# Kernel tuning notes

Hardware: AMD Instinct MI355X
Metric: run time of the kernel (lower is better)

The kernel has to match this reference:

```python
import jax, jax.numpy as jnp
import numpy as np


def setup_inputs() -> dict:
    key = jax.random.key(0)
    ks = jax.random.split(key, 16)
    B, S, D, H = 32, 2048, 512, 512
    s = 1.0 / np.sqrt(H)
    inp = {
        "x": jax.random.normal(ks[0], (B, H), jnp.float32),
        "context": jax.random.normal(ks[1], (B, S, D), jnp.float32),
        "mask": jnp.zeros((B, S), jnp.bool_),  # False = valid position
        "Wi": jax.random.normal(ks[2], (H, H), jnp.float32) * s,
        "bi": jax.random.normal(ks[3], (H,), jnp.float32) * s,
        "Wc0": jax.random.normal(ks[4], (H, D), jnp.float32) * s,
        "bc0": jax.random.normal(ks[5], (H,), jnp.float32) * s,
        "Wc1": jax.random.normal(ks[6], (H, D), jnp.float32) * s,
        "bc1": jax.random.normal(ks[7], (H,), jnp.float32) * s,
        "Wc2": jax.random.normal(ks[8], (H, D), jnp.float32) * s,
        "bc2": jax.random.normal(ks[9], (H,), jnp.float32) * s,
        "Wc3": jax.random.normal(ks[10], (H, D), jnp.float32) * s,
        "bc3": jax.random.normal(ks[11], (H,), jnp.float32) * s,
        "V": jax.random.uniform(ks[12], (H,), jnp.float32, -s, s),
    }
    return inp


def reference(x, context, mask, Wi, bi, Wc0, bc0, Wc1, bc1, Wc2, bc2, Wc3, bc3, V):
    # mask: True = masked out in the original API; module flips it first.
    valid = ~mask  # [B, S], True = keep

    inp = (x @ Wi.T + bi)[:, :, None]  # [B, H, 1]

    def proj(W, b):
        # Conv1d(D, H, kernel=1) on context.permute(0,2,1) == token-wise GEMM
        return jnp.einsum("bsd,hd->bhs", context, W) + b[None, :, None]  # [B, H, S]

    ctx = jnp.concatenate(
        [proj(Wc0, bc0), proj(Wc1, bc1), proj(Wc2, bc2), proj(Wc3, bc3)], axis=2
    )  # [B, H, 4S]

    t = jnp.tanh(inp + ctx)                      # [B, H, 4S]
    att = jnp.einsum("h,bhs->bs", V, t)          # bmm(V[B,1,H], t).squeeze(1)
    att = 10.0 * jnp.tanh(att)                   # [B, 4S]

    valid4 = jnp.tile(valid, (1, 4))             # mask.repeat(1, 4)
    att = jnp.where(valid4, att, -jnp.inf)
    # torch.no_grad() around the masked fill detaches the rest of the graph
    att = jax.lax.stop_gradient(att)

    ans = jax.nn.softmax(att, axis=1)            # [B, 4S]
    p = jnp.max(ans, axis=1)
    indices = jnp.argmax(ans, axis=1)
    return indices[:, None], p[:, None], mask
```

## Files before the change

kernel.cpp:

```cpp
#include <hip/hip_runtime.h>
#include <math.h>

typedef __bf16 bf16x8 __attribute__((ext_vector_type(8)));
typedef float f32x4 __attribute__((ext_vector_type(4)));
typedef short short8v __attribute__((ext_vector_type(8)));

#define MARGIN 0.01f
#define NCAND 32

#define WAITL  do { asm volatile("s_waitcnt lgkmcnt(0)" ::: "memory"); __builtin_amdgcn_sched_barrier(0); } while (0)
#define WAITV0 do { asm volatile("s_waitcnt vmcnt(0)" ::: "memory"); __builtin_amdgcn_sched_barrier(0); } while (0)
#define BARR   do { __builtin_amdgcn_s_barrier(); __builtin_amdgcn_sched_barrier(0); } while (0)

__device__ __forceinline__ unsigned short f2bf(float f) {
  unsigned u = __float_as_uint(f);
  u += 0x7fffu + ((u >> 16) & 1u);
  return (unsigned short)(u >> 16);
}
__device__ __forceinline__ float tanh_fast(float x) {
  float e = __builtin_amdgcn_exp2f(x * 2.885390081777927f);
  return 1.f - 2.f * __builtin_amdgcn_rcpf(e + 1.f);
}
__device__ __forceinline__ void gl_lds16(const void* g, void* l) {
  __builtin_amdgcn_global_load_lds(
      (const __attribute__((address_space(1))) unsigned int*)g,
      (__attribute__((address_space(3))) unsigned int*)l, 16, 0, 0);
}
__device__ __forceinline__ float dpp_row_reduce(float v) {
  int x;
  x = __builtin_amdgcn_update_dpp(0, __builtin_bit_cast(int, v), 0x118, 0xf, 0xf, true);
  v += __builtin_bit_cast(float, x);
  x = __builtin_amdgcn_update_dpp(0, __builtin_bit_cast(int, v), 0x114, 0xf, 0xf, true);
  v += __builtin_bit_cast(float, x);
  x = __builtin_amdgcn_update_dpp(0, __builtin_bit_cast(int, v), 0x112, 0xf, 0xf, true);
  v += __builtin_bit_cast(float, x);
  x = __builtin_amdgcn_update_dpp(0, __builtin_bit_cast(int, v), 0x111, 0xf, 0xf, true);
  v += __builtin_bit_cast(float, x);
  return v;
}

__global__ __launch_bounds__(256) void prep_all_k(
    const float* __restrict__ ctx, const float* __restrict__ x,
    const float* __restrict__ Wi, const float* __restrict__ bi,
    const float* __restrict__ w0, const float* __restrict__ w1,
    const float* __restrict__ w2, const float* __restrict__ w3,
    short* __restrict__ Chi, short* __restrict__ Whi, float* __restrict__ inp,
    int ctx_blocks) {
  int bid = blockIdx.x;
  if (bid < ctx_blocks) {
    int gid = bid * 256 + threadIdx.x;
    int c = gid & 3, row = (gid >> 2) & 127, TK = gid >> 9;
    int MT = TK >> 4, KS = TK & 15;
    size_t m = (size_t)MT * 128 + row;
    int k = KS * 32 + c * 8;
    float f[8];
    *(float4*)&f[0] = *(const float4*)(ctx + m * 512 + k);
    *(float4*)&f[4] = *(const float4*)(ctx + m * 512 + k + 4);
    short8v hv;
    #pragma unroll
    for (int i = 0; i < 8; ++i) hv[i] = (short)f2bf(f[i]);
    *(short8v*)(Chi + (size_t)gid * 8) = hv;
  } else if (bid < ctx_blocks + 512) {
    int gid = (bid - ctx_blocks) * 256 + threadIdx.x;
    int c = gid & 3, row = (gid >> 2) & 511, TK = gid >> 11;
    int TN = TK >> 4, KS = TK & 15;
    const float* w = (TN == 0) ? w0 : (TN == 1) ? w1 : (TN == 2) ? w2 : w3;
    const float* src = w + (size_t)row * 512 + KS * 32 + c * 8;
    float f[8];
    *(float4*)&f[0] = *(const float4*)(src);
    *(float4*)&f[4] = *(const float4*)(src + 4);
    short8v hv;
    #pragma unroll
    for (int i = 0; i < 8; ++i) hv[i] = (short)f2bf(f[i]);
    *(short8v*)(Whi + (size_t)gid * 8) = hv;
  } else {
    int gid = (bid - ctx_blocks - 512) * 256 + threadIdx.x;
    int b = gid >> 9, h = gid & 511;
    const float* xr = x + b * 512;
    const float* wr = Wi + h * 512;
    float acc = bi[h];
    #pragma unroll 4
    for (int k = 0; k < 512; k += 4) {
      float4 xv = *(const float4*)(xr + k);
      float4 wv = *(const float4*)(wr + k);
      acc += xv.x * wv.x + xv.y * wv.y + xv.z * wv.z + xv.w * wv.w;
    }
    inp[gid] = acc;
  }
}

template<bool PRESPLIT>
__global__ __launch_bounds__(1024, 4) void gemm_att_k(
    const float* __restrict__ ctx, const short* __restrict__ Chi,
    const short* __restrict__ Whi,
    const float* __restrict__ inp,
    const float* __restrict__ bc0, const float* __restrict__ bc1,
    const float* __restrict__ bc2, const float* __restrict__ bc3,
    const float* __restrict__ V, float* __restrict__ att) {
  __shared__ __align__(16) short smem[2][20480];

  const int t = threadIdx.x;
  int d = blockIdx.x + (blockIdx.y << 3);
  int work = (d & 7) * 256 + (d >> 3);
  int mt = work >> 2, nt = work & 3;
  int b = mt >> 4;
  const float* bc = (nt == 0) ? bc0 : (nt == 1) ? bc1 : (nt == 2) ? bc2 : bc3;

  auto stageA = [&](int tile, int slot) {
    if (t < 512)
      gl_lds16(Chi + (((size_t)mt * 16 + tile) << 12) + t * 8, &smem[slot][t * 8]);
  };
  auto stageB = [&](int tile, int slot) {
    const short* gB = Whi + (((size_t)nt * 16 + tile) << 14) + t * 8;
    short* lB = &smem[slot][4096 + t * 8];
    gl_lds16(gB,        lB);
    gl_lds16(gB + 8192, lB + 8192);
  };
  auto stageA_reg = [&](int tile, int slot) {
    if (t < 512) {
      int c = t & 3, r = t >> 2;
      const float* src = ctx + ((size_t)mt * 128 + r) * 512 + tile * 32 + c * 8;
      float f[8];
      *(float4*)&f[0] = *(const float4*)src;
      *(float4*)&f[4] = *(const float4*)(src + 4);
      short8v hv;
      #pragma unroll
      for (int i = 0; i < 8; ++i) hv[i] = (short)f2bf(f[i]);
      *(short8v*)(&smem[slot][r * 32 + c * 8]) = hv;
    }
  };

  f32x4 acc[4][4];
  #pragma unroll
  for (int i = 0; i < 4; ++i)
    #pragma unroll
    for (int j = 0; j < 4; ++j) acc[i][j] = (f32x4){0.f, 0.f, 0.f, 0.f};

  const int lane = t & 63, wid = t >> 6;
  const int wr = wid >> 3, wc = wid & 7;
  const int fr = lane & 15, fq = lane >> 4;
  const int abase = (wr * 64 + fr) * 32 + fq * 8;
  const int bbase = 4096 + (wc * 64 + fr) * 32 + fq * 8;

  if constexpr (PRESPLIT) { stageA(0, 0); stageB(0, 0); WAITV0; }
  else { stageA_reg(0, 0); stageB(0, 0); WAITV0; WAITL; }
  BARR;

  #pragma unroll 2
  for (int tt = 0; tt < 16; ++tt) {
    const int slot = tt & 1;
    const short* s = &smem[slot][0];
    bf16x8 a[4], bv[4];
    #pragma unroll
    for (int mi = 0; mi < 4; ++mi) a[mi] = *(const bf16x8*)(s + abase + mi * 512);
    #pragma unroll
    for (int ni = 0; ni < 4; ++ni) bv[ni] = *(const bf16x8*)(s + bbase + ni * 512);
    if (tt < 15) {
      if constexpr (PRESPLIT) { stageA(tt + 1, slot ^ 1); }
      stageB(tt + 1, slot ^ 1);
    }
    WAITL;
    __builtin_amdgcn_s_setprio(1);
    #pragma unroll
    for (int mi = 0; mi < 4; ++mi)
      #pragma unroll
      for (int ni = 0; ni < 4; ++ni)
        acc[mi][ni] = __builtin_amdgcn_mfma_f32_16x16x32_bf16(a[mi], bv[ni], acc[mi][ni], 0, 0, 0);
    __builtin_amdgcn_s_setprio(0);
    __builtin_amdgcn_sched_barrier(0);
    if (tt < 15) {
      if constexpr (!PRESPLIT) { stageA_reg(tt + 1, slot ^ 1); WAITL; }
      WAITV0;
    }
    BARR;
  }

  float vV[4], vP[4];
  #pragma unroll
  for (int ni = 0; ni < 4; ++ni) {
    int j = wc * 64 + ni * 16 + fr;
    vV[ni] = V[j];
    vP[ni] = inp[b * 512 + j] + bc[j];
  }
  size_t abatt = (size_t)b * 8192 + (size_t)nt * 2048;
  #pragma unroll
  for (int mi = 0; mi < 4; ++mi) {
    #pragma unroll
    for (int r = 0; r < 4; ++r) {
      float sum = 0.f;
      #pragma unroll
      for (int ni = 0; ni < 4; ++ni)
        sum += vV[ni] * tanh_fast(vP[ni] + acc[mi][ni][r]);
      sum = dpp_row_reduce(sum);
      if (fr == 15) {
        int s2 = (mt & 15) * 128 + wr * 64 + mi * 16 + fq * 4 + r;
        atomicAdd(&att[abatt + s2], sum);
      }
    }
  }
}

__global__ __launch_bounds__(1024) void tail_k(const float* __restrict__ att,
    const unsigned char* __restrict__ mask, const float* __restrict__ ctx,
    const float* __restrict__ Wc0, const float* __restrict__ Wc1,
    const float* __restrict__ Wc2, const float* __restrict__ Wc3,
    const float* __restrict__ bc0, const float* __restrict__ bc1,
    const float* __restrict__ bc2, const float* __restrict__ bc3,
    const float* __restrict__ inp, const float* __restrict__ V,
    float* __restrict__ out) {
  int b = blockIdx.x, t = threadIdx.x;
  __shared__ float sred[1024];
  __shared__ float sctx[512];
  __shared__ int scnt;
  __shared__ int scand_j[NCAND];
  __shared__ float scand_a[NCAND];
  __shared__ float sexact[NCAND];

  if (t == 0) scnt = 0;
  float bm = -1e30f;
  for (int j = t; j < 8192; j += 1024) {
    if (mask[b * 2048 + (j & 2047)]) continue;
    bm = fmaxf(bm, att[(size_t)b * 8192 + j]);
  }
  sred[t] = bm;
  __syncthreads();
  for (int s2 = 512; s2 > 0; s2 >>= 1) {
    if (t < s2) sred[t] = fmaxf(sred[t], sred[t + s2]);
    __syncthreads();
  }
  float mx = sred[0];
  float Lref = 10.f * tanhf(mx);
  __syncthreads();
  float se = 0.f;
  for (int j = t; j < 8192; j += 1024) {
    if (mask[b * 2048 + (j & 2047)]) continue;
    float a = att[(size_t)b * 8192 + j];
    se += expf(10.f * tanhf(a) - Lref);
    if (a >= mx - MARGIN) {
      int slot = atomicAdd(&scnt, 1);
      if (slot < NCAND) { scand_j[slot] = j; scand_a[slot] = a; }
    }
  }
  sred[t] = se;
  __syncthreads();
  for (int s2 = 512; s2 > 0; s2 >>= 1) {
    if (t < s2) sred[t] += sred[t + s2];
    __syncthreads();
  }
  float den = sred[0];
  int n = min(scnt, NCAND);
  for (int j = t; j < 2048; j += 1024)
    out[64 + b * 2048 + j] = mask[b * 2048 + j] ? 1.0f : 0.0f;
  for (int i = 0; i < n; ++i) {
    int jj = scand_j[i];
    int g = jj >> 11, s = jj & 2047;
    const float* W  = (g == 0) ? Wc0 : (g == 1) ? Wc1 : (g == 2) ? Wc2 : Wc3;
    const float* bc = (g == 0) ? bc0 : (g == 1) ? bc1 : (g == 2) ? bc2 : bc3;
    const float* cr = ctx + ((size_t)b * 2048 + s) * 512;
    __syncthreads();
    if (t < 512) sctx[t] = cr[t];
    __syncthreads();
    float total = 0.f;
    if (t < 512) {
      const float* wrp = W + (size_t)t * 512;
      float acc = 0.f;
      #pragma unroll 4
      for (int k = 0; k < 512; k += 4) {
        float4 wv = *(const float4*)(wrp + k);
        acc += wv.x * sctx[k] + wv.y * sctx[k + 1] + wv.z * sctx[k + 2] + wv.w * sctx[k + 3];
      }
      total = V[t] * tanhf(inp[b * 512 + t] + bc[t] + acc);
    }
    sred[t] = total;
    __syncthreads();
    for (int s2 = 512; s2 > 0; s2 >>= 1) {
      if (t < s2) sred[t] += sred[t + s2];
      __syncthreads();
    }
    if (t == 0) sexact[i] = sred[0];
  }
  __syncthreads();
  if (t == 0) {
    float dd = den, best = -1e30f;
    int bj = 0x7fffffff;
    for (int i = 0; i < n; ++i) {
      float e = sexact[i];
      int j = scand_j[i];
      dd += expf(10.f * tanhf(e) - Lref) - expf(10.f * tanhf(scand_a[i]) - Lref);
      if (e > best || (e == best && j < bj)) { best = e; bj = j; }
    }
    out[b] = (float)bj;
    out[32 + b] = expf(10.f * tanhf(best) - Lref) / dd;
  }
}

extern "C" void kernel_launch(void* const* d_in, const int* in_sizes, int n_in,
                              void* d_out, int out_size, void* d_ws, size_t ws_size,
                              hipStream_t stream) {
  const float* x    = (const float*)d_in[0];
  const float* ctx  = (const float*)d_in[1];
  const unsigned char* mask = (const unsigned char*)d_in[2];
  const float* Wi   = (const float*)d_in[3];
  const float* bi   = (const float*)d_in[4];
  const float* Wc0  = (const float*)d_in[5];
  const float* bc0  = (const float*)d_in[6];
  const float* Wc1  = (const float*)d_in[7];
  const float* bc1  = (const float*)d_in[8];
  const float* Wc2  = (const float*)d_in[9];
  const float* bc2  = (const float*)d_in[10];
  const float* Wc3  = (const float*)d_in[11];
  const float* bc3  = (const float*)d_in[12];
  const float* V    = (const float*)d_in[13];
  float* out = (float*)d_out;

  float* inp = (float*)d_ws;
  float* att = inp + 16384;
  short* Whi = (short*)(att + 262144);
  short* Chi = Whi + 1048576;
  size_t need = (size_t)((char*)(Chi + 33554432) - (char*)d_ws);
  bool presplit = ws_size >= need;

  hipMemsetAsync(att, 0, 262144 * sizeof(float), stream);
  if (presplit) {
    prep_all_k<<<16960, 256, 0, stream>>>(ctx, x, Wi, bi,
        Wc0, Wc1, Wc2, Wc3, Chi, Whi, inp, 16384);
    gemm_att_k<true><<<dim3(8, 256), 1024, 0, stream>>>(ctx, Chi, Whi,
        inp, bc0, bc1, bc2, bc3, V, att);
  } else {
    prep_all_k<<<576, 256, 0, stream>>>(ctx, x, Wi, bi,
        Wc0, Wc1, Wc2, Wc3, nullptr, Whi, inp, 0);
    gemm_att_k<false><<<dim3(8, 256), 1024, 0, stream>>>(ctx, nullptr, Whi,
        inp, bc0, bc1, bc2, bc3, V, att);
  }
  tail_k<<<32, 1024, 0, stream>>>(att, mask, ctx, Wc0, Wc1, Wc2, Wc3,
      bc0, bc1, bc2, bc3, inp, V, out);
}
```

Measured before the change: 303.0 us.

## Load fp32 context directly to LDS and convert in-kernel, dropping bf16 presplit pass

Removes the separate pass that converted the whole context tensor to bf16 in global memory. The GEMM now streams fp32 context tiles straight into LDS with async global-to-LDS loads, using an XOR-swizzled layout, and converts them to bf16 with packed cvt instructions just before the MFMAs. The pipeline goes from double to triple buffering with a partial vmcnt wait. This avoids writing and re-reading a large intermediate, but it doubles LDS traffic for the A operand and uses much more shared memory per block, which may lower occupancy.

```diff
diff --git a/kernel.cpp b/kernel.cpp
--- a/kernel.cpp
+++ b/kernel.cpp
@@ -10,6 +10,7 @@
 
 #define WAITL  do { asm volatile("s_waitcnt lgkmcnt(0)" ::: "memory"); __builtin_amdgcn_sched_barrier(0); } while (0)
 #define WAITV0 do { asm volatile("s_waitcnt vmcnt(0)" ::: "memory"); __builtin_amdgcn_sched_barrier(0); } while (0)
+#define WAITV3 do { asm volatile("s_waitcnt vmcnt(3)" ::: "memory"); __builtin_amdgcn_sched_barrier(0); } while (0)
 #define BARR   do { __builtin_amdgcn_s_barrier(); __builtin_amdgcn_sched_barrier(0); } while (0)
 
 __device__ __forceinline__ unsigned short f2bf(float f) {
@@ -25,6 +26,11 @@
   __builtin_amdgcn_global_load_lds(
       (const __attribute__((address_space(1))) unsigned int*)g,
       (__attribute__((address_space(3))) unsigned int*)l, 16, 0, 0);
+}
+__device__ __forceinline__ int cvt_pk_bf16(float lo, float hi) {
+  int r;
+  asm("v_cvt_pk_bf16_f32 %0, %1, %2" : "=v"(r) : "v"(lo), "v"(hi));
+  return r;
 }
 __device__ __forceinline__ float dpp_row_reduce(float v) {
   int x;
@@ -39,29 +45,15 @@
   return v;
 }
 
-__global__ __launch_bounds__(256) void prep_all_k(
-    const float* __restrict__ ctx, const float* __restrict__ x,
-    const float* __restrict__ Wi, const float* __restrict__ bi,
+__global__ __launch_bounds__(256) void prep_small_k(
+    const float* __restrict__ x, const float* __restrict__ Wi,
+    const float* __restrict__ bi,
     const float* __restrict__ w0, const float* __restrict__ w1,
     const float* __restrict__ w2, const float* __restrict__ w3,
-    short* __restrict__ Chi, short* __restrict__ Whi, float* __restrict__ inp,
-    int ctx_blocks) {
+    short* __restrict__ Whi, float* __restrict__ inp) {
   int bid = blockIdx.x;
-  if (bid < ctx_blocks) {
+  if (bid < 512) {
     int gid = bid * 256 + threadIdx.x;
-    int c = gid & 3, row = (gid >> 2) & 127, TK = gid >> 9;
-    int MT = TK >> 4, KS = TK & 15;
-    size_t m = (size_t)MT * 128 + row;
-    int k = KS * 32 + c * 8;
-    float f[8];
-    *(float4*)&f[0] = *(const float4*)(ctx + m * 512 + k);
-    *(float4*)&f[4] = *(const float4*)(ctx + m * 512 + k + 4);
-    short8v hv;
-    #pragma unroll
-    for (int i = 0; i < 8; ++i) hv[i] = (short)f2bf(f[i]);
-    *(short8v*)(Chi + (size_t)gid * 8) = hv;
-  } else if (bid < ctx_blocks + 512) {
-    int gid = (bid - ctx_blocks) * 256 + threadIdx.x;
     int c = gid & 3, row = (gid >> 2) & 511, TK = gid >> 11;
     int TN = TK >> 4, KS = TK & 15;
     const float* w = (TN == 0) ? w0 : (TN == 1) ? w1 : (TN == 2) ? w2 : w3;
@@ -74,7 +66,7 @@
     for (int i = 0; i < 8; ++i) hv[i] = (short)f2bf(f[i]);
     *(short8v*)(Whi + (size_t)gid * 8) = hv;
   } else {
-    int gid = (bid - ctx_blocks - 512) * 256 + threadIdx.x;
+    int gid = (bid - 512) * 256 + threadIdx.x;
     int b = gid >> 9, h = gid & 511;
     const float* xr = x + b * 512;
     const float* wr = Wi + h * 512;
@@ -89,15 +81,13 @@
   }
 }
 
-template<bool PRESPLIT>
 __global__ __launch_bounds__(1024, 4) void gemm_att_k(
-    const float* __restrict__ ctx, const short* __restrict__ Chi,
-    const short* __restrict__ Whi,
+    const float* __restrict__ ctx, const short* __restrict__ Whi,
     const float* __restrict__ inp,
     const float* __restrict__ bc0, const float* __restrict__ bc1,
     const float* __restrict__ bc2, const float* __restrict__ bc3,
     const float* __restrict__ V, float* __restrict__ att) {
-  __shared__ __align__(16) short smem[2][20480];
+  __shared__ __align__(16) char smem[3][49152];
 
   const int t = threadIdx.x;
   int d = blockIdx.x + (blockIdx.y << 3);
@@ -106,29 +96,19 @@
   int b = mt >> 4;
   const float* bc = (nt == 0) ? bc0 : (nt == 1) ? bc1 : (nt == 2) ? bc2 : bc3;
 
+  const int ar = t >> 3, apos = t & 7;
+  const int aq = apos ^ (ar & 7);
+  const float* aSrc = ctx + ((size_t)mt * 128 + ar) * 512 + aq * 4;
+
   auto stageA = [&](int tile, int slot) {
-    if (t < 512)
-      gl_lds16(Chi + (((size_t)mt * 16 + tile) << 12) + t * 8, &smem[slot][t * 8]);
+    gl_lds16(aSrc + tile * 32, (float*)&smem[slot][0] + t * 4);
   };
   auto stageB = [&](int tile, int slot) {
     const short* gB = Whi + (((size_t)nt * 16 + tile) << 14) + t * 8;
-    short* lB = &smem[slot][4096 + t * 8];
+    short* lB = (short*)&smem[slot][16384] + t * 8;
     gl_lds16(gB,        lB);
     gl_lds16(gB + 8192, lB + 8192);
   };
-  auto stageA_reg = [&](int tile, int slot) {
-    if (t < 512) {
-      int c = t & 3, r = t >> 2;
-      const float* src = ctx + ((size_t)mt * 128 + r) * 512 + tile * 32 + c * 8;
-      float f[8];
-      *(float4*)&f[0] = *(const float4*)src;
-      *(float4*)&f[4] = *(const float4*)(src + 4);
-      short8v hv;
-      #pragma unroll
-      for (int i = 0; i < 8; ++i) hv[i] = (short)f2bf(f[i]);
-      *(short8v*)(&smem[slot][r * 32 + c * 8]) = hv;
-    }
-  };
 
   f32x4 acc[4][4];
   #pragma unroll
@@ -139,26 +119,36 @@
   const int lane = t & 63, wid = t >> 6;
   const int wr = wid >> 3, wc = wid & 7;
   const int fr = lane & 15, fq = lane >> 4;
-  const int abase = (wr * 64 + fr) * 32 + fq * 8;
-  const int bbase = 4096 + (wc * 64 + fr) * 32 + fq * 8;
-
-  if constexpr (PRESPLIT) { stageA(0, 0); stageB(0, 0); WAITV0; }
-  else { stageA_reg(0, 0); stageB(0, 0); WAITV0; WAITL; }
+  const int s7 = fr & 7;
+  const int p0 = (fq * 2) ^ s7;
+  const int bbase = (wc * 64 + fr) * 32 + fq * 8;
+
+  stageA(0, 0); stageB(0, 0);
+  stageA(1, 1); stageB(1, 1);
+  WAITV3;
   BARR;
 
-  #pragma unroll 2
+  #pragma unroll
   for (int tt = 0; tt < 16; ++tt) {
-    const int slot = tt & 1;
-    const short* s = &smem[slot][0];
+    const int slot = tt % 3;
+    const float* As = (const float*)&smem[slot][0];
+    const short* Bs = (const short*)&smem[slot][16384];
+    if (tt < 14) { stageA(tt + 2, (tt + 2) % 3); stageB(tt + 2, (tt + 2) % 3); }
     bf16x8 a[4], bv[4];
     #pragma unroll
-    for (int mi = 0; mi < 4; ++mi) a[mi] = *(const bf16x8*)(s + abase + mi * 512);
-    #pragma unroll
-    for (int ni = 0; ni < 4; ++ni) bv[ni] = *(const bf16x8*)(s + bbase + ni * 512);
-    if (tt < 15) {
-      if constexpr (PRESPLIT) { stageA(tt + 1, slot ^ 1); }
-      stageB(tt + 1, slot ^ 1);
-    }
+    for (int mi = 0; mi < 4; ++mi) {
+      int rowb = (wr * 64 + mi * 16 + fr) * 32;
+      f32x4 c0 = *(const f32x4*)(As + rowb + p0 * 4);
+      f32x4 c1 = *(const f32x4*)(As + rowb + (p0 ^ 1) * 4);
+      int4 w;
+      w.x = cvt_pk_bf16(c0[0], c0[1]);
+      w.y = cvt_pk_bf16(c0[2], c0[3]);
+      w.z = cvt_pk_bf16(c1[0], c1[1]);
+      w.w = cvt_pk_bf16(c1[2], c1[3]);
+      a[mi] = __builtin_bit_cast(bf16x8, w);
+    }
+    #pragma unroll
+    for (int ni = 0; ni < 4; ++ni) bv[ni] = *(const bf16x8*)(Bs + bbase + ni * 512);
     WAITL;
     __builtin_amdgcn_s_setprio(1);
     #pragma unroll
@@ -168,10 +158,8 @@
         acc[mi][ni] = __builtin_amdgcn_mfma_f32_16x16x32_bf16(a[mi], bv[ni], acc[mi][ni], 0, 0, 0);
     __builtin_amdgcn_s_setprio(0);
     __builtin_amdgcn_sched_barrier(0);
-    if (tt < 15) {
-      if constexpr (!PRESPLIT) { stageA_reg(tt + 1, slot ^ 1); WAITL; }
-      WAITV0;
-    }
+    if (tt < 14) { WAITV3; }
+    else if (tt == 14) { WAITV0; }
     BARR;
   }
 
@@ -316,22 +304,11 @@
   float* inp = (float*)d_ws;
   float* att = inp + 16384;
   short* Whi = (short*)(att + 262144);
-  short* Chi = Whi + 1048576;
-  size_t need = (size_t)((char*)(Chi + 33554432) - (char*)d_ws);
-  bool presplit = ws_size >= need;
 
   hipMemsetAsync(att, 0, 262144 * sizeof(float), stream);
-  if (presplit) {
-    prep_all_k<<<16960, 256, 0, stream>>>(ctx, x, Wi, bi,
-        Wc0, Wc1, Wc2, Wc3, Chi, Whi, inp, 16384);
-    gemm_att_k<true><<<dim3(8, 256), 1024, 0, stream>>>(ctx, Chi, Whi,
-        inp, bc0, bc1, bc2, bc3, V, att);
-  } else {
-    prep_all_k<<<576, 256, 0, stream>>>(ctx, x, Wi, bi,
-        Wc0, Wc1, Wc2, Wc3, nullptr, Whi, inp, 0);
-    gemm_att_k<false><<<dim3(8, 256), 1024, 0, stream>>>(ctx, nullptr, Whi,
-        inp, bc0, bc1, bc2, bc3, V, att);
-  }
+  prep_small_k<<<576, 256, 0, stream>>>(x, Wi, bi, Wc0, Wc1, Wc2, Wc3, Whi, inp);
+  gemm_att_k<<<dim3(8, 256), 1024, 0, stream>>>(ctx, Whi,
+      inp, bc0, bc1, bc2, bc3, V, att);
   tail_k<<<32, 1024, 0, stream>>>(att, mask, ctx, Wc0, Wc1, Wc2, Wc3,
       bc0, bc1, bc2, bc3, inp, V, out);
 }
```

Measured after the change: 291.5 us. 3.8% less time.
